# Kernel optimization log

Measured on AMD Instinct MI355X. Metric: run time of the kernel, lower is better.

## Reference

```python
import jax, jax.numpy as jnp
import numpy as np

D_MODEL = 768
MIMO_RANK = 4


def setup_inputs() -> dict:
    key = jax.random.key(0)
    ks = jax.random.split(key, 6)
    B, T, D, R = 2, 2048, D_MODEL, MIMO_RANK
    x = jax.random.normal(ks[0], (B, T, D), dtype=jnp.float32)
    norm_w = jnp.ones((D,), dtype=jnp.float32)
    W_in = jax.random.normal(ks[1], (D * R * 2, D), dtype=jnp.float32) * 0.02
    W_out = jax.random.normal(ks[2], (D, D), dtype=jnp.float32) * 0.02
    a_param = jax.random.normal(ks[3], (D, R, 2), dtype=jnp.float32) * 0.12
    b_param = jax.random.normal(ks[4], (D, R, 2), dtype=jnp.float32) * 0.15
    c_param = jax.random.normal(ks[5], (D, R, 2), dtype=jnp.float32) * 0.15
    return {"x": x, "norm_w": norm_w, "W_in": W_in, "W_out": W_out,
            "a_param": a_param, "b_param": b_param, "c_param": c_param}


def reference(x, norm_w, W_in, W_out, a_param, b_param, c_param):
    B, T, D = x.shape
    R = a_param.shape[1]
    # RMSNorm
    xn = x * jax.lax.rsqrt(jnp.mean(x * x, axis=-1, keepdims=True) + 1e-6) * norm_w
    # in_proj -> interleaved complex MIMO input u: [B,T,D,R,2]
    u = (xn @ W_in.T).reshape(B, T, D, R, 2)
    # coefficients (tanh-bounded; |a| scaled by 0.97 for stability)
    a = jnp.tanh(a_param) * 0.97
    b = jnp.tanh(b_param)
    c = jnp.tanh(c_param)
    ac = jax.lax.complex(a[..., 0], a[..., 1])  # [D,R]
    bc = jax.lax.complex(b[..., 0], b[..., 1])
    cc = jax.lax.complex(c[..., 0], c[..., 1])
    uc = jax.lax.complex(u[..., 0], u[..., 1])  # [B,T,D,R]
    # linear complex recurrence s_t = a * s_{t-1} + b * u_t, zero init state,
    # parallelized with an associative scan over time.
    bu = bc[None, None] * uc
    A = jnp.broadcast_to(ac[None, None], bu.shape)

    def comb(l, r):
        return (l[0] * r[0], r[0] * l[1] + r[1])

    _, s = jax.lax.associative_scan(comb, (A, bu), axis=1)  # [B,T,D,R] complex
    # output mix: real part of c * h, summed over MIMO rank -> [B,T,D]
    y = jnp.real(cc[None, None] * s).sum(axis=-1)
    return y @ W_out.T
```

## Files before the change

### kernel.cpp

```cpp
#include <hip/hip_runtime.h>
#include <hip/hip_bf16.h>
#include <stdint.h>

#define BATCH 2
#define TT 2048
#define DM 768
#define RR 4
#define M_TOK 4096
#define NFEAT 6144
#define NCH 6144
#define CHUNK 64
#define NCHUNK 32

typedef __attribute__((ext_vector_type(8))) short short8;
typedef __attribute__((ext_vector_type(4))) float float4v;

__device__ inline float bf2f(uint32_t bits16) {
    union { uint32_t u; float f; } x; x.u = bits16 << 16; return x.f;
}

typedef const __attribute__((address_space(1))) void* gptr_t;
typedef __attribute__((address_space(3))) void* lptr_t;

__device__ inline void async_ld16(const void* g, void* l) {
    __builtin_amdgcn_global_load_lds((gptr_t)(uintptr_t)g, (lptr_t)(uintptr_t)l,
                                     16, 0, 0);
}

__device__ inline void store_c(__hip_bfloat16* C, size_t idx, float v) {
    C[idx] = __float2bfloat16(v);
}
__device__ inline void store_c(float* C, size_t idx, float v) { C[idx] = v; }

__device__ inline uint2 pack4bf(float a, float b, float c, float d) {
    union { __hip_bfloat16 h[4]; uint2 u; } o;
    o.h[0] = __float2bfloat16(a); o.h[1] = __float2bfloat16(b);
    o.h[2] = __float2bfloat16(c); o.h[3] = __float2bfloat16(d);
    return o.u;
}

__global__ __launch_bounds__(256) void prep_rms(
    const float* __restrict__ x, const float* __restrict__ w,
    const float* __restrict__ W_in, const float* __restrict__ W_out,
    const float* __restrict__ ap, const float* __restrict__ bp,
    const float* __restrict__ cp,
    __hip_bfloat16* __restrict__ xn,
    __hip_bfloat16* __restrict__ Win_bf, __hip_bfloat16* __restrict__ Wout_bf,
    float2* __restrict__ ac, float2* __restrict__ bc,
    float2* __restrict__ cc, float2* __restrict__ aL) {
    int bid = blockIdx.x;
    int tid = threadIdx.x;
    if (bid < M_TOK) {
        __shared__ float wsum[3];
        float4 v = make_float4(0.f, 0.f, 0.f, 0.f);
        if (tid < 192) v = ((const float4*)(x + (size_t)bid * DM))[tid];
        float ss = v.x * v.x + v.y * v.y + v.z * v.z + v.w * v.w;
        #pragma unroll
        for (int o = 1; o < 64; o <<= 1) ss += __shfl_xor(ss, o);
        if (tid < 192 && (tid & 63) == 0) wsum[tid >> 6] = ss;
        __syncthreads();
        if (tid < 192) {
            float tot = wsum[0] + wsum[1] + wsum[2];
            float scale = rsqrtf(tot * (1.f / DM) + 1e-6f);
            float4 wv = ((const float4*)w)[tid];
            ((uint2*)(xn + (size_t)bid * DM))[tid] =
                pack4bf(v.x * scale * wv.x, v.y * scale * wv.y,
                        v.z * scale * wv.z, v.w * scale * wv.w);
        }
        return;
    }
    const int N1 = NFEAT * DM / 4;
    const int N2 = DM * DM / 4;
    int i = (bid - M_TOK) * 256 + tid;
    if (i < N1) {
        float4 v = ((const float4*)W_in)[i];
        ((uint2*)Win_bf)[i] = pack4bf(v.x, v.y, v.z, v.w);
    } else if (i < N1 + N2) {
        int k = i - N1;
        float4 v = ((const float4*)W_out)[k];
        ((uint2*)Wout_bf)[k] = pack4bf(v.x, v.y, v.z, v.w);
    }
    if (i < DM * RR) {
        float ar = tanhf(ap[2 * i])     * 0.97f;
        float ai = tanhf(ap[2 * i + 1]) * 0.97f;
        ac[i] = make_float2(ar, ai);
        bc[i] = make_float2(tanhf(bp[2 * i]), tanhf(bp[2 * i + 1]));
        cc[i] = make_float2(tanhf(cp[2 * i]), tanhf(cp[2 * i + 1]));
        float xr = ar, xi = ai;
        #pragma unroll
        for (int k = 0; k < 6; ++k) {
            float nr = xr * xr - xi * xi;
            float ni = 2.f * xr * xi;
            xr = nr; xi = ni;
        }
        aL[i] = make_float2(xr, xi);
    }
}

template <int BM, int BN, int BK, typename OutT>
__device__ inline void gemm_body(
    const __hip_bfloat16* __restrict__ A, const __hip_bfloat16* __restrict__ B,
    OutT* __restrict__ C, int K, int ldc, int n0base) {
    constexpr int MI = BM / 32;
    constexpr int NJ = BN / 32;
    constexpr int CPR = BK / 8;
    __shared__ __attribute__((aligned(16))) __hip_bfloat16 lA[BM * BK];
    __shared__ __attribute__((aligned(16))) __hip_bfloat16 lB[BN * BK];
    const int tid  = threadIdx.x;
    const int lane = tid & 63;
    const int wave = tid >> 6;
    const int quad = lane >> 4;
    const int l15  = lane & 15;
    const int wm = (wave >> 1) * (BM / 2);
    const int wn = (wave & 1) * (BN / 2);
    const int m0 = blockIdx.y * BM;
    const int n0 = n0base + blockIdx.x * BN;

    float4v acc[MI][NJ] = {};

    for (int k0 = 0; k0 < K; k0 += BK) {
        __syncthreads();
        #pragma unroll
        for (int it = 0; it < BM * CPR / 256; ++it) {
            int p = it * 256 + tid;
            int row = p / CPR;
            int cg = (p & (CPR - 1)) ^ (row & (CPR - 1));
            async_ld16(A + (size_t)(m0 + row) * K + k0 + cg * 8, lA + p * 8);
        }
        #pragma unroll
        for (int it = 0; it < BN * CPR / 256; ++it) {
            int p = it * 256 + tid;
            int row = p / CPR;
            int cg = (p & (CPR - 1)) ^ (row & (CPR - 1));
            async_ld16(B + (size_t)(n0 + row) * K + k0 + cg * 8, lB + p * 8);
        }
        __syncthreads();
        #pragma unroll
        for (int s = 0; s < BK / 32; ++s) {
            short8 af[MI], bfr[NJ];
            #pragma unroll
            for (int i = 0; i < MI; ++i) {
                int r = wm + i * 16 + l15;
                int c = (s * 4 + quad) ^ (r & (CPR - 1));
                af[i] = *(const short8*)(lA + r * BK + c * 8);
            }
            #pragma unroll
            for (int j = 0; j < NJ; ++j) {
                int r = wn + j * 16 + l15;
                int c = (s * 4 + quad) ^ (r & (CPR - 1));
                bfr[j] = *(const short8*)(lB + r * BK + c * 8);
            }
            #pragma unroll
            for (int i = 0; i < MI; ++i)
                #pragma unroll
                for (int j = 0; j < NJ; ++j)
                    acc[i][j] = __builtin_amdgcn_mfma_f32_16x16x32_bf16(
                        af[i], bfr[j], acc[i][j], 0, 0, 0);
        }
    }
    #pragma unroll
    for (int i = 0; i < MI; ++i)
        #pragma unroll
        for (int j = 0; j < NJ; ++j)
            #pragma unroll
            for (int rg = 0; rg < 4; ++rg) {
                int row = m0 + wm + i * 16 + quad * 4 + rg;
                int col = n0 + wn + j * 16 + l15;
                store_c(C, (size_t)row * ldc + col, acc[i][j][rg]);
            }
}

__global__ __launch_bounds__(256) void gemm_in_a(
    const __hip_bfloat16* __restrict__ A, const __hip_bfloat16* __restrict__ B,
    __hip_bfloat16* __restrict__ C, int K) {
    gemm_body<128, 128, 64, __hip_bfloat16>(A, B, C, K, NFEAT, 0);
}
__global__ __launch_bounds__(256) void gemm_in_b(
    const __hip_bfloat16* __restrict__ A, const __hip_bfloat16* __restrict__ B,
    __hip_bfloat16* __restrict__ C, int K) {
    gemm_body<128, 128, 64, __hip_bfloat16>(A, B, C, K, NFEAT, NFEAT / 2);
}

__global__ __launch_bounds__(256) void gemm_out(
    const __hip_bfloat16* __restrict__ A, const __hip_bfloat16* __restrict__ B,
    float* __restrict__ C, int K) {
    gemm_body<64, 64, 128, float>(A, B, C, K, DM, 0);
}

__device__ inline void cstep(float& sr, float& si, float2 a, float2 bb,
                             uint32_t uw) {
    float ur = bf2f(uw & 0xffffu), ui = bf2f(uw >> 16);
    float tr = bb.x * ur - bb.y * ui;
    float ti = bb.x * ui + bb.y * ur;
    float nr = a.x * sr - a.y * si + tr;
    float ni = a.x * si + a.y * sr + ti;
    sr = nr; si = ni;
}

__global__ __launch_bounds__(256) void scan_passA(
    const uint4* __restrict__ u4,
    const float2* __restrict__ ac, const float2* __restrict__ bc,
    float2* __restrict__ chunkEnd) {
    int g = blockIdx.x * 256 + threadIdx.x;
    int j = blockIdx.y;
    int b = g >= DM;
    int d = g - b * DM;
    int cb = d * RR;
    float2 a0 = ac[cb], a1 = ac[cb + 1], a2 = ac[cb + 2], a3 = ac[cb + 3];
    float2 b0 = bc[cb], b1 = bc[cb + 1], b2 = bc[cb + 2], b3 = bc[cb + 3];
    float s0r = 0, s0i = 0, s1r = 0, s1i = 0;
    float s2r = 0, s2i = 0, s3r = 0, s3i = 0;
    size_t base = ((size_t)(b * TT + j * CHUNK)) * DM + d;
    #pragma unroll 4
    for (int i = 0; i < CHUNK; ++i) {
        uint4 uw = u4[base + (size_t)i * DM];
        cstep(s0r, s0i, a0, b0, uw.x);
        cstep(s1r, s1i, a1, b1, uw.y);
        cstep(s2r, s2i, a2, b2, uw.z);
        cstep(s3r, s3i, a3, b3, uw.w);
    }
    size_t eb = (size_t)j * NCH + b * (DM * RR) + cb;
    chunkEnd[eb]     = make_float2(s0r, s0i);
    chunkEnd[eb + 1] = make_float2(s1r, s1i);
    chunkEnd[eb + 2] = make_float2(s2r, s2i);
    chunkEnd[eb + 3] = make_float2(s3r, s3i);
}

__global__ __launch_bounds__(256) void scan_passC(
    const uint4* __restrict__ u4,
    const float2* __restrict__ ac, const float2* __restrict__ bc,
    const float2* __restrict__ cc, const float2* __restrict__ aLp,
    const float2* __restrict__ chunkEnd,
    __hip_bfloat16* __restrict__ y) {
    int g = blockIdx.x * 256 + threadIdx.x;
    int j = blockIdx.y;
    int b = g >= DM;
    int d = g - b * DM;
    int cb = d * RR;
    float2 a0 = ac[cb], a1 = ac[cb + 1], a2 = ac[cb + 2], a3 = ac[cb + 3];
    float2 b0 = bc[cb], b1 = bc[cb + 1], b2 = bc[cb + 2], b3 = bc[cb + 3];
    float2 c0 = cc[cb], c1 = cc[cb + 1], c2 = cc[cb + 2], c3 = cc[cb + 3];
    float2 aL0 = aLp[cb], aL1 = aLp[cb + 1], aL2 = aLp[cb + 2], aL3 = aLp[cb + 3];
    float s0r = 0, s0i = 0, s1r = 0, s1i = 0;
    float s2r = 0, s2i = 0, s3r = 0, s3i = 0;
    for (int jj = 0; jj < j; ++jj) {
        size_t eb = (size_t)jj * NCH + b * (DM * RR) + cb;
        float2 e0 = chunkEnd[eb],     e1 = chunkEnd[eb + 1];
        float2 e2 = chunkEnd[eb + 2], e3 = chunkEnd[eb + 3];
        float nr, ni;
        nr = aL0.x * s0r - aL0.y * s0i + e0.x; ni = aL0.x * s0i + aL0.y * s0r + e0.y; s0r = nr; s0i = ni;
        nr = aL1.x * s1r - aL1.y * s1i + e1.x; ni = aL1.x * s1i + aL1.y * s1r + e1.y; s1r = nr; s1i = ni;
        nr = aL2.x * s2r - aL2.y * s2i + e2.x; ni = aL2.x * s2i + aL2.y * s2r + e2.y; s2r = nr; s2i = ni;
        nr = aL3.x * s3r - aL3.y * s3i + e3.x; ni = aL3.x * s3i + aL3.y * s3r + e3.y; s3r = nr; s3i = ni;
    }
    size_t base = ((size_t)(b * TT + j * CHUNK)) * DM + d;
    #pragma unroll 4
    for (int i = 0; i < CHUNK; ++i) {
        uint4 uw = u4[base + (size_t)i * DM];
        cstep(s0r, s0i, a0, b0, uw.x);
        cstep(s1r, s1i, a1, b1, uw.y);
        cstep(s2r, s2i, a2, b2, uw.z);
        cstep(s3r, s3i, a3, b3, uw.w);
        float yv = c0.x * s0r - c0.y * s0i + c1.x * s1r - c1.y * s1i
                 + c2.x * s2r - c2.y * s2i + c3.x * s3r - c3.y * s3i;
        y[base + (size_t)i * DM] = __float2bfloat16(yv);
    }
}

extern "C" void kernel_launch(void* const* d_in, const int* in_sizes, int n_in,
                              void* d_out, int out_size, void* d_ws,
                              size_t ws_size, hipStream_t stream) {
    const float* x      = (const float*)d_in[0];
    const float* norm_w = (const float*)d_in[1];
    const float* W_in   = (const float*)d_in[2];
    const float* W_out  = (const float*)d_in[3];
    const float* a_p    = (const float*)d_in[4];
    const float* b_p    = (const float*)d_in[5];
    const float* c_p    = (const float*)d_in[6];
    float* out = (float*)d_out;

    char* ws = (char*)d_ws;
    size_t off = 0;
    auto alloc = [&](size_t bytes) {
        void* p = ws + off;
        off += (bytes + 255) & ~(size_t)255;
        return p;
    };
    __hip_bfloat16* Win_bf  = (__hip_bfloat16*)alloc((size_t)NFEAT * DM * 2);
    __hip_bfloat16* Wout_bf = (__hip_bfloat16*)alloc((size_t)DM * DM * 2);
    __hip_bfloat16* xn      = (__hip_bfloat16*)alloc((size_t)M_TOK * DM * 2);
    __hip_bfloat16* u       = (__hip_bfloat16*)alloc((size_t)M_TOK * NFEAT * 2);
    __hip_bfloat16* y       = (__hip_bfloat16*)alloc((size_t)M_TOK * DM * 2);
    float2* ac = (float2*)alloc((size_t)DM * RR * 8);
    float2* bc = (float2*)alloc((size_t)DM * RR * 8);
    float2* cc = (float2*)alloc((size_t)DM * RR * 8);
    float2* aL = (float2*)alloc((size_t)DM * RR * 8);
    float2* chunkEnd = (float2*)alloc((size_t)NCHUNK * NCH * 8);

    {
        int cast_blocks = ((NFEAT * DM + DM * DM) / 4 + 255) / 256;
        prep_rms<<<M_TOK + cast_blocks, 256, 0, stream>>>(
            x, norm_w, W_in, W_out, a_p, b_p, c_p,
            xn, Win_bf, Wout_bf, ac, bc, cc, aL);
    }
    gemm_in_a<<<dim3(NFEAT / 256, M_TOK / 128), 256, 0, stream>>>(
        xn, Win_bf, u, DM);
    gemm_in_b<<<dim3(NFEAT / 256, M_TOK / 128), 256, 0, stream>>>(
        xn, Win_bf, u, DM);
    scan_passA<<<dim3(BATCH * DM / 256, NCHUNK), 256, 0, stream>>>(
        (const uint4*)u, ac, bc, chunkEnd);
    scan_passC<<<dim3(BATCH * DM / 256, NCHUNK), 256, 0, stream>>>(
        (const uint4*)u, ac, bc, cc, aL, chunkEnd, y);
    gemm_out<<<dim3(DM / 64, M_TOK / 64), 256, 0, stream>>>(
        y, Wout_bf, out, DM);
}
```

Baseline: 202.1 us.

## Fuse chunk-local scan pass into input-projection GEMM epilogue

The input-projection GEMM now stages its bf16 output tile in shared memory. Half the threads then run the chunk-local complex recurrence over 64 timesteps for each channel and write the chunk end states directly. This removes the separate scan_passA kernel, which had to re-read the whole u tensor from global memory, and merges the two half-GEMM launches into one. The cost is a serial 64-step scan inside the GEMM tail, run by only 128 threads, plus extra LDS traffic and syncs per block.

```diff
diff --git a/kernel.cpp b/kernel.cpp
--- a/kernel.cpp
+++ b/kernel.cpp
@@ -27,16 +27,21 @@
                                      16, 0, 0);
 }
 
-__device__ inline void store_c(__hip_bfloat16* C, size_t idx, float v) {
-    C[idx] = __float2bfloat16(v);
-}
-__device__ inline void store_c(float* C, size_t idx, float v) { C[idx] = v; }
-
 __device__ inline uint2 pack4bf(float a, float b, float c, float d) {
     union { __hip_bfloat16 h[4]; uint2 u; } o;
     o.h[0] = __float2bfloat16(a); o.h[1] = __float2bfloat16(b);
     o.h[2] = __float2bfloat16(c); o.h[3] = __float2bfloat16(d);
     return o.u;
+}
+
+__device__ inline void cstep(float& sr, float& si, float2 a, float2 bb,
+                             uint32_t uw) {
+    float ur = bf2f(uw & 0xffffu), ui = bf2f(uw >> 16);
+    float tr = bb.x * ur - bb.y * ui;
+    float ti = bb.x * ui + bb.y * ur;
+    float nr = a.x * sr - a.y * si + tr;
+    float ni = a.x * si + a.y * sr + ti;
+    sr = nr; si = ni;
 }
 
 __global__ __launch_bounds__(256) void prep_rms(
@@ -97,13 +102,113 @@
     }
 }
 
-template <int BM, int BN, int BK, typename OutT>
-__device__ inline void gemm_body(
+__global__ __launch_bounds__(256) void gemm_in_scan(
     const __hip_bfloat16* __restrict__ A, const __hip_bfloat16* __restrict__ B,
-    OutT* __restrict__ C, int K, int ldc, int n0base) {
-    constexpr int MI = BM / 32;
-    constexpr int NJ = BN / 32;
-    constexpr int CPR = BK / 8;
+    __hip_bfloat16* __restrict__ C,
+    const float2* __restrict__ ac, const float2* __restrict__ bc,
+    float2* __restrict__ chunkEnd) {
+    constexpr int BM = 128, BN = 128, BK = 64;
+    constexpr int MI = BM / 32, NJ = BN / 32, CPR = BK / 8;
+    constexpr int K = DM;
+    __shared__ __attribute__((aligned(16))) __hip_bfloat16 smem[BM * BK + BN * BK];
+    __hip_bfloat16* lA = smem;
+    __hip_bfloat16* lB = smem + BM * BK;
+    const int tid  = threadIdx.x;
+    const int lane = tid & 63;
+    const int wave = tid >> 6;
+    const int quad = lane >> 4;
+    const int l15  = lane & 15;
+    const int wm = (wave >> 1) * (BM / 2);
+    const int wn = (wave & 1) * (BN / 2);
+    const int m0 = blockIdx.y * BM;
+    const int n0 = blockIdx.x * BN;
+
+    float4v acc[MI][NJ] = {};
+
+    for (int k0 = 0; k0 < K; k0 += BK) {
+        __syncthreads();
+        #pragma unroll
+        for (int it = 0; it < BM * CPR / 256; ++it) {
+            int p = it * 256 + tid;
+            int row = p / CPR;
+            int cg = (p & (CPR - 1)) ^ (row & (CPR - 1));
+            async_ld16(A + (size_t)(m0 + row) * K + k0 + cg * 8, lA + p * 8);
+        }
+        #pragma unroll
+        for (int it = 0; it < BN * CPR / 256; ++it) {
+            int p = it * 256 + tid;
+            int row = p / CPR;
+            int cg = (p & (CPR - 1)) ^ (row & (CPR - 1));
+            async_ld16(B + (size_t)(n0 + row) * K + k0 + cg * 8, lB + p * 8);
+        }
+        __syncthreads();
+        #pragma unroll
+        for (int s = 0; s < BK / 32; ++s) {
+            short8 af[MI], bfr[NJ];
+            #pragma unroll
+            for (int i = 0; i < MI; ++i) {
+                int r = wm + i * 16 + l15;
+                int c = (s * 4 + quad) ^ (r & (CPR - 1));
+                af[i] = *(const short8*)(lA + r * BK + c * 8);
+            }
+            #pragma unroll
+            for (int j = 0; j < NJ; ++j) {
+                int r = wn + j * 16 + l15;
+                int c = (s * 4 + quad) ^ (r & (CPR - 1));
+                bfr[j] = *(const short8*)(lB + r * BK + c * 8);
+            }
+            #pragma unroll
+            for (int i = 0; i < MI; ++i)
+                #pragma unroll
+                for (int j = 0; j < NJ; ++j)
+                    acc[i][j] = __builtin_amdgcn_mfma_f32_16x16x32_bf16(
+                        af[i], bfr[j], acc[i][j], 0, 0, 0);
+        }
+    }
+    __syncthreads();
+    #pragma unroll
+    for (int i = 0; i < MI; ++i)
+        #pragma unroll
+        for (int j = 0; j < NJ; ++j)
+            #pragma unroll
+            for (int rg = 0; rg < 4; ++rg) {
+                int row = wm + i * 16 + quad * 4 + rg;
+                int col = wn + j * 16 + l15;
+                float v = acc[i][j][rg];
+                __hip_bfloat16 h = __float2bfloat16(v);
+                C[(size_t)(m0 + row) * NFEAT + n0 + col] = h;
+                int pc = (((col >> 3) ^ (row & 15)) << 3) | (col & 7);
+                smem[row * BN + pc] = h;
+            }
+    __syncthreads();
+    if (tid < 128) {
+        int ch    = tid & 63;
+        int chunk = tid >> 6;
+        int rem = n0 / 2 + ch;
+        int b = m0 >= TT;
+        int jg = ((m0 & (TT - 1)) >> 6) + chunk;
+        float2 a = ac[rem], bb = bc[rem];
+        float sr = 0.f, si = 0.f;
+        int col = 2 * ch;
+        int cchunk = col >> 3, cin = col & 7;
+        int t0 = chunk * 64;
+        #pragma unroll 8
+        for (int t = 0; t < 64; ++t) {
+            int row = t0 + t;
+            int pc = ((cchunk ^ (row & 15)) << 3) | cin;
+            uint32_t val = *(const uint32_t*)(smem + row * BN + pc);
+            cstep(sr, si, a, bb, val);
+        }
+        chunkEnd[(size_t)jg * NCH + b * (DM * RR) + rem] = make_float2(sr, si);
+    }
+}
+
+__global__ __launch_bounds__(256) void gemm_out(
+    const __hip_bfloat16* __restrict__ A, const __hip_bfloat16* __restrict__ B,
+    float* __restrict__ C) {
+    constexpr int BM = 64, BN = 64, BK = 128;
+    constexpr int MI = BM / 32, NJ = BN / 32, CPR = BK / 8;
+    constexpr int K = DM;
     __shared__ __attribute__((aligned(16))) __hip_bfloat16 lA[BM * BK];
     __shared__ __attribute__((aligned(16))) __hip_bfloat16 lB[BN * BK];
     const int tid  = threadIdx.x;
@@ -114,7 +219,7 @@
     const int wm = (wave >> 1) * (BM / 2);
     const int wn = (wave & 1) * (BN / 2);
     const int m0 = blockIdx.y * BM;
-    const int n0 = n0base + blockIdx.x * BN;
+    const int n0 = blockIdx.x * BN;
 
     float4v acc[MI][NJ] = {};
 
@@ -166,64 +271,8 @@
             for (int rg = 0; rg < 4; ++rg) {
                 int row = m0 + wm + i * 16 + quad * 4 + rg;
                 int col = n0 + wn + j * 16 + l15;
-                store_c(C, (size_t)row * ldc + col, acc[i][j][rg]);
-            }
-}
-
-__global__ __launch_bounds__(256) void gemm_in_a(
-    const __hip_bfloat16* __restrict__ A, const __hip_bfloat16* __restrict__ B,
-    __hip_bfloat16* __restrict__ C, int K) {
-    gemm_body<128, 128, 64, __hip_bfloat16>(A, B, C, K, NFEAT, 0);
-}
-__global__ __launch_bounds__(256) void gemm_in_b(
-    const __hip_bfloat16* __restrict__ A, const __hip_bfloat16* __restrict__ B,
-    __hip_bfloat16* __restrict__ C, int K) {
-    gemm_body<128, 128, 64, __hip_bfloat16>(A, B, C, K, NFEAT, NFEAT / 2);
-}
-
-__global__ __launch_bounds__(256) void gemm_out(
-    const __hip_bfloat16* __restrict__ A, const __hip_bfloat16* __restrict__ B,
-    float* __restrict__ C, int K) {
-    gemm_body<64, 64, 128, float>(A, B, C, K, DM, 0);
-}
-
-__device__ inline void cstep(float& sr, float& si, float2 a, float2 bb,
-                             uint32_t uw) {
-    float ur = bf2f(uw & 0xffffu), ui = bf2f(uw >> 16);
-    float tr = bb.x * ur - bb.y * ui;
-    float ti = bb.x * ui + bb.y * ur;
-    float nr = a.x * sr - a.y * si + tr;
-    float ni = a.x * si + a.y * sr + ti;
-    sr = nr; si = ni;
-}
-
-__global__ __launch_bounds__(256) void scan_passA(
-    const uint4* __restrict__ u4,
-    const float2* __restrict__ ac, const float2* __restrict__ bc,
-    float2* __restrict__ chunkEnd) {
-    int g = blockIdx.x * 256 + threadIdx.x;
-    int j = blockIdx.y;
-    int b = g >= DM;
-    int d = g - b * DM;
-    int cb = d * RR;
-    float2 a0 = ac[cb], a1 = ac[cb + 1], a2 = ac[cb + 2], a3 = ac[cb + 3];
-    float2 b0 = bc[cb], b1 = bc[cb + 1], b2 = bc[cb + 2], b3 = bc[cb + 3];
-    float s0r = 0, s0i = 0, s1r = 0, s1i = 0;
-    float s2r = 0, s2i = 0, s3r = 0, s3i = 0;
-    size_t base = ((size_t)(b * TT + j * CHUNK)) * DM + d;
-    #pragma unroll 4
-    for (int i = 0; i < CHUNK; ++i) {
-        uint4 uw = u4[base + (size_t)i * DM];
-        cstep(s0r, s0i, a0, b0, uw.x);
-        cstep(s1r, s1i, a1, b1, uw.y);
-        cstep(s2r, s2i, a2, b2, uw.z);
-        cstep(s3r, s3i, a3, b3, uw.w);
-    }
-    size_t eb = (size_t)j * NCH + b * (DM * RR) + cb;
-    chunkEnd[eb]     = make_float2(s0r, s0i);
-    chunkEnd[eb + 1] = make_float2(s1r, s1i);
-    chunkEnd[eb + 2] = make_float2(s2r, s2i);
-    chunkEnd[eb + 3] = make_float2(s3r, s3i);
+                C[(size_t)row * DM + col] = acc[i][j][rg];
+            }
 }
 
 __global__ __launch_bounds__(256) void scan_passC(
@@ -303,14 +352,10 @@
             x, norm_w, W_in, W_out, a_p, b_p, c_p,
             xn, Win_bf, Wout_bf, ac, bc, cc, aL);
     }
-    gemm_in_a<<<dim3(NFEAT / 256, M_TOK / 128), 256, 0, stream>>>(
-        xn, Win_bf, u, DM);
-    gemm_in_b<<<dim3(NFEAT / 256, M_TOK / 128), 256, 0, stream>>>(
-        xn, Win_bf, u, DM);
-    scan_passA<<<dim3(BATCH * DM / 256, NCHUNK), 256, 0, stream>>>(
-        (const uint4*)u, ac, bc, chunkEnd);
+    gemm_in_scan<<<dim3(NFEAT / 128, M_TOK / 128), 256, 0, stream>>>(
+        xn, Win_bf, u, ac, bc, chunkEnd);
     scan_passC<<<dim3(BATCH * DM / 256, NCHUNK), 256, 0, stream>>>(
         (const uint4*)u, ac, bc, cc, aL, chunkEnd, y);
     gemm_out<<<dim3(DM / 64, M_TOK / 64), 256, 0, stream>>>(
-        y, Wout_bf, out, DM);
-}
+        y, Wout_bf, out);
+}
```

Result: faster. 195.6 us (-3.2%).

## Compute local scan outputs once and fix up with carried state instead of rescanning u

Applied to the files above, without the earlier changes.

The first scan pass now writes a local per-chunk output y_local (zero initial state) alongside the chunk end states. The second pass no longer re-reads the large bf16 u tensor to rerun the recurrence. Instead it adds the carry-in term Re(c·a^(i+1)·k), advanced by one complex multiply per step, to y_local. This swaps a second full read of u (4096x6144 bf16) for a write plus a read of an fp32 4096x768 buffer. The two split in_proj GEMM launches are also merged into one launch with 256x128 tiles, which raises register and LDS use per block.

```diff
diff --git a/kernel.cpp b/kernel.cpp
--- a/kernel.cpp
+++ b/kernel.cpp
@@ -37,6 +37,20 @@
     o.h[0] = __float2bfloat16(a); o.h[1] = __float2bfloat16(b);
     o.h[2] = __float2bfloat16(c); o.h[3] = __float2bfloat16(d);
     return o.u;
+}
+
+__device__ inline float2 cmul(float2 a, float2 b) {
+    return make_float2(a.x * b.x - a.y * b.y, a.x * b.y + a.y * b.x);
+}
+
+__device__ inline void cstep(float& sr, float& si, float2 a, float2 bb,
+                             uint32_t uw) {
+    float ur = bf2f(uw & 0xffffu), ui = bf2f(uw >> 16);
+    float tr = bb.x * ur - bb.y * ui;
+    float ti = bb.x * ui + bb.y * ur;
+    float nr = a.x * sr - a.y * si + tr;
+    float ni = a.x * si + a.y * sr + ti;
+    sr = nr; si = ni;
 }
 
 __global__ __launch_bounds__(256) void prep_rms(
@@ -100,7 +114,7 @@
 template <int BM, int BN, int BK, typename OutT>
 __device__ inline void gemm_body(
     const __hip_bfloat16* __restrict__ A, const __hip_bfloat16* __restrict__ B,
-    OutT* __restrict__ C, int K, int ldc, int n0base) {
+    OutT* __restrict__ C, int K, int ldc) {
     constexpr int MI = BM / 32;
     constexpr int NJ = BN / 32;
     constexpr int CPR = BK / 8;
@@ -114,7 +128,7 @@
     const int wm = (wave >> 1) * (BM / 2);
     const int wn = (wave & 1) * (BN / 2);
     const int m0 = blockIdx.y * BM;
-    const int n0 = n0base + blockIdx.x * BN;
+    const int n0 = blockIdx.x * BN;
 
     float4v acc[MI][NJ] = {};
 
@@ -170,36 +184,23 @@
             }
 }
 
-__global__ __launch_bounds__(256) void gemm_in_a(
+__global__ __launch_bounds__(256) void gemm_in_bigm(
     const __hip_bfloat16* __restrict__ A, const __hip_bfloat16* __restrict__ B,
     __hip_bfloat16* __restrict__ C, int K) {
-    gemm_body<128, 128, 64, __hip_bfloat16>(A, B, C, K, NFEAT, 0);
-}
-__global__ __launch_bounds__(256) void gemm_in_b(
-    const __hip_bfloat16* __restrict__ A, const __hip_bfloat16* __restrict__ B,
-    __hip_bfloat16* __restrict__ C, int K) {
-    gemm_body<128, 128, 64, __hip_bfloat16>(A, B, C, K, NFEAT, NFEAT / 2);
+    gemm_body<256, 128, 64, __hip_bfloat16>(A, B, C, K, NFEAT);
 }
 
 __global__ __launch_bounds__(256) void gemm_out(
     const __hip_bfloat16* __restrict__ A, const __hip_bfloat16* __restrict__ B,
     float* __restrict__ C, int K) {
-    gemm_body<64, 64, 128, float>(A, B, C, K, DM, 0);
-}
-
-__device__ inline void cstep(float& sr, float& si, float2 a, float2 bb,
-                             uint32_t uw) {
-    float ur = bf2f(uw & 0xffffu), ui = bf2f(uw >> 16);
-    float tr = bb.x * ur - bb.y * ui;
-    float ti = bb.x * ui + bb.y * ur;
-    float nr = a.x * sr - a.y * si + tr;
-    float ni = a.x * si + a.y * sr + ti;
-    sr = nr; si = ni;
-}
-
-__global__ __launch_bounds__(256) void scan_passA(
+    gemm_body<64, 64, 128, float>(A, B, C, K, DM);
+}
+
+__global__ __launch_bounds__(256) void scan_local(
     const uint4* __restrict__ u4,
     const float2* __restrict__ ac, const float2* __restrict__ bc,
+    const float2* __restrict__ cc,
+    float* __restrict__ y_local,
     float2* __restrict__ chunkEnd) {
     int g = blockIdx.x * 256 + threadIdx.x;
     int j = blockIdx.y;
@@ -208,6 +209,7 @@
     int cb = d * RR;
     float2 a0 = ac[cb], a1 = ac[cb + 1], a2 = ac[cb + 2], a3 = ac[cb + 3];
     float2 b0 = bc[cb], b1 = bc[cb + 1], b2 = bc[cb + 2], b3 = bc[cb + 3];
+    float2 c0 = cc[cb], c1 = cc[cb + 1], c2 = cc[cb + 2], c3 = cc[cb + 3];
     float s0r = 0, s0i = 0, s1r = 0, s1i = 0;
     float s2r = 0, s2i = 0, s3r = 0, s3i = 0;
     size_t base = ((size_t)(b * TT + j * CHUNK)) * DM + d;
@@ -218,6 +220,9 @@
         cstep(s1r, s1i, a1, b1, uw.y);
         cstep(s2r, s2i, a2, b2, uw.z);
         cstep(s3r, s3i, a3, b3, uw.w);
+        float yv = c0.x * s0r - c0.y * s0i + c1.x * s1r - c1.y * s1i
+                 + c2.x * s2r - c2.y * s2i + c3.x * s3r - c3.y * s3i;
+        y_local[base + (size_t)i * DM] = yv;
     }
     size_t eb = (size_t)j * NCH + b * (DM * RR) + cb;
     chunkEnd[eb]     = make_float2(s0r, s0i);
@@ -226,11 +231,10 @@
     chunkEnd[eb + 3] = make_float2(s3r, s3i);
 }
 
-__global__ __launch_bounds__(256) void scan_passC(
-    const uint4* __restrict__ u4,
-    const float2* __restrict__ ac, const float2* __restrict__ bc,
-    const float2* __restrict__ cc, const float2* __restrict__ aLp,
-    const float2* __restrict__ chunkEnd,
+__global__ __launch_bounds__(256) void scan_fix(
+    const float* __restrict__ y_local,
+    const float2* __restrict__ ac, const float2* __restrict__ cc,
+    const float2* __restrict__ aLp, const float2* __restrict__ chunkEnd,
     __hip_bfloat16* __restrict__ y) {
     int g = blockIdx.x * 256 + threadIdx.x;
     int j = blockIdx.y;
@@ -238,32 +242,29 @@
     int d = g - b * DM;
     int cb = d * RR;
     float2 a0 = ac[cb], a1 = ac[cb + 1], a2 = ac[cb + 2], a3 = ac[cb + 3];
-    float2 b0 = bc[cb], b1 = bc[cb + 1], b2 = bc[cb + 2], b3 = bc[cb + 3];
-    float2 c0 = cc[cb], c1 = cc[cb + 1], c2 = cc[cb + 2], c3 = cc[cb + 3];
     float2 aL0 = aLp[cb], aL1 = aLp[cb + 1], aL2 = aLp[cb + 2], aL3 = aLp[cb + 3];
-    float s0r = 0, s0i = 0, s1r = 0, s1i = 0;
-    float s2r = 0, s2i = 0, s3r = 0, s3i = 0;
+    float2 k0 = make_float2(0, 0), k1 = k0, k2 = k0, k3 = k0;
     for (int jj = 0; jj < j; ++jj) {
         size_t eb = (size_t)jj * NCH + b * (DM * RR) + cb;
         float2 e0 = chunkEnd[eb],     e1 = chunkEnd[eb + 1];
         float2 e2 = chunkEnd[eb + 2], e3 = chunkEnd[eb + 3];
         float nr, ni;
-        nr = aL0.x * s0r - aL0.y * s0i + e0.x; ni = aL0.x * s0i + aL0.y * s0r + e0.y; s0r = nr; s0i = ni;
-        nr = aL1.x * s1r - aL1.y * s1i + e1.x; ni = aL1.x * s1i + aL1.y * s1r + e1.y; s1r = nr; s1i = ni;
-        nr = aL2.x * s2r - aL2.y * s2i + e2.x; ni = aL2.x * s2i + aL2.y * s2r + e2.y; s2r = nr; s2i = ni;
-        nr = aL3.x * s3r - aL3.y * s3i + e3.x; ni = aL3.x * s3i + aL3.y * s3r + e3.y; s3r = nr; s3i = ni;
-    }
+        nr = aL0.x * k0.x - aL0.y * k0.y + e0.x; ni = aL0.x * k0.y + aL0.y * k0.x + e0.y; k0 = make_float2(nr, ni);
+        nr = aL1.x * k1.x - aL1.y * k1.y + e1.x; ni = aL1.x * k1.y + aL1.y * k1.x + e1.y; k1 = make_float2(nr, ni);
+        nr = aL2.x * k2.x - aL2.y * k2.y + e2.x; ni = aL2.x * k2.y + aL2.y * k2.x + e2.y; k2 = make_float2(nr, ni);
+        nr = aL3.x * k3.x - aL3.y * k3.y + e3.x; ni = aL3.x * k3.y + aL3.y * k3.x + e3.y; k3 = make_float2(nr, ni);
+    }
+    float2 q0 = cmul(cmul(cc[cb],     k0), a0);
+    float2 q1 = cmul(cmul(cc[cb + 1], k1), a1);
+    float2 q2 = cmul(cmul(cc[cb + 2], k2), a2);
+    float2 q3 = cmul(cmul(cc[cb + 3], k3), a3);
     size_t base = ((size_t)(b * TT + j * CHUNK)) * DM + d;
     #pragma unroll 4
     for (int i = 0; i < CHUNK; ++i) {
-        uint4 uw = u4[base + (size_t)i * DM];
-        cstep(s0r, s0i, a0, b0, uw.x);
-        cstep(s1r, s1i, a1, b1, uw.y);
-        cstep(s2r, s2i, a2, b2, uw.z);
-        cstep(s3r, s3i, a3, b3, uw.w);
-        float yv = c0.x * s0r - c0.y * s0i + c1.x * s1r - c1.y * s1i
-                 + c2.x * s2r - c2.y * s2i + c3.x * s3r - c3.y * s3i;
+        float yv = y_local[base + (size_t)i * DM] + q0.x + q1.x + q2.x + q3.x;
         y[base + (size_t)i * DM] = __float2bfloat16(yv);
+        q0 = cmul(q0, a0); q1 = cmul(q1, a1);
+        q2 = cmul(q2, a2); q3 = cmul(q3, a3);
     }
 }
 
@@ -290,6 +291,7 @@
     __hip_bfloat16* Wout_bf = (__hip_bfloat16*)alloc((size_t)DM * DM * 2);
     __hip_bfloat16* xn      = (__hip_bfloat16*)alloc((size_t)M_TOK * DM * 2);
     __hip_bfloat16* u       = (__hip_bfloat16*)alloc((size_t)M_TOK * NFEAT * 2);
+    float*          y_local = (float*)alloc((size_t)M_TOK * DM * 4);
     __hip_bfloat16* y       = (__hip_bfloat16*)alloc((size_t)M_TOK * DM * 2);
     float2* ac = (float2*)alloc((size_t)DM * RR * 8);
     float2* bc = (float2*)alloc((size_t)DM * RR * 8);
@@ -303,14 +305,12 @@
             x, norm_w, W_in, W_out, a_p, b_p, c_p,
             xn, Win_bf, Wout_bf, ac, bc, cc, aL);
     }
-    gemm_in_a<<<dim3(NFEAT / 256, M_TOK / 128), 256, 0, stream>>>(
+    gemm_in_bigm<<<dim3(NFEAT / 128, M_TOK / 256), 256, 0, stream>>>(
         xn, Win_bf, u, DM);
-    gemm_in_b<<<dim3(NFEAT / 256, M_TOK / 128), 256, 0, stream>>>(
-        xn, Win_bf, u, DM);
-    scan_passA<<<dim3(BATCH * DM / 256, NCHUNK), 256, 0, stream>>>(
-        (const uint4*)u, ac, bc, chunkEnd);
-    scan_passC<<<dim3(BATCH * DM / 256, NCHUNK), 256, 0, stream>>>(
-        (const uint4*)u, ac, bc, cc, aL, chunkEnd, y);
+    scan_local<<<dim3(BATCH * DM / 256, NCHUNK), 256, 0, stream>>>(
+        (const uint4*)u, ac, bc, cc, y_local, chunkEnd);
+    scan_fix<<<dim3(BATCH * DM / 256, NCHUNK), 256, 0, stream>>>(
+        y_local, ac, cc, aL, chunkEnd, y);
     gemm_out<<<dim3(DM / 64, M_TOK / 64), 256, 0, stream>>>(
         y, Wout_bf, out, DM);
 }
```

Result: slower. 217.3 us (+7.5%).
